# Kernel optimization log

Hardware: AMD Instinct MI355X
Metric: run time of the kernel (lower is better)

## Reference

```python
import math
import jax, jax.numpy as jnp
import numpy as np

SAMPLE_RATE = 16000
N_BANDS = 3
_F_DARK = jnp.array([270.0, 800.0, 2300.0], dtype=jnp.float32)
_F_NEUTRAL = jnp.array([500.0, 1500.0, 2500.0], dtype=jnp.float32)
_F_BRIGHT = jnp.array([730.0, 2100.0, 3000.0], dtype=jnp.float32)
_Q_DARK = jnp.array([5.0, 5.0, 5.0], dtype=jnp.float32)
_Q_NEUTRAL = jnp.array([8.0, 8.0, 8.0], dtype=jnp.float32)
_Q_BRIGHT = jnp.array([12.0, 12.0, 12.0], dtype=jnp.float32)


def _interpolate_formants(level):
    # level: [B] in [0,1] -> freqs, qs: [B, n_bands]
    t_low = jnp.clip(level * 2.0, 0.0, 1.0)[:, None]
    t_high = jnp.clip((level - 0.5) * 2.0, 0.0, 1.0)[:, None]
    use_high = (level >= 0.5)[:, None]
    freqs_lo = (1.0 - t_low) * _F_DARK + t_low * _F_NEUTRAL
    qs_lo = (1.0 - t_low) * _Q_DARK + t_low * _Q_NEUTRAL
    freqs_hi = (1.0 - t_high) * _F_NEUTRAL + t_high * _F_BRIGHT
    qs_hi = (1.0 - t_high) * _Q_NEUTRAL + t_high * _Q_BRIGHT
    freqs = jnp.where(use_high, freqs_hi, freqs_lo)
    qs = jnp.where(use_high, qs_hi, qs_lo)
    return freqs, qs


def _biquad_bandpass_coeffs(freq_hz, q):
    # freq_hz, q: [B, n_bands] -> coeffs each [B, n_bands]; b1 is 0
    omega = (2.0 * math.pi / SAMPLE_RATE) * freq_hz
    sin_o = jnp.sin(omega)
    cos_o = jnp.cos(omega)
    alpha = sin_o / (2.0 * jnp.maximum(q, 0.5))
    a0 = 1.0 + alpha
    b0 = alpha / a0
    b2 = -alpha / a0
    a1 = (-2.0 * cos_o) / a0
    a2 = (1.0 - alpha) / a0
    return b0, b2, a1, a2


def setup_inputs() -> dict:
    key = jax.random.key(0)
    k1, k2 = jax.random.split(key)
    B, S = 256, 131072
    audio = jax.random.normal(k1, (B, S), dtype=jnp.float32)
    resonance_level = jax.random.uniform(k2, (B,), dtype=jnp.float32)
    return {"audio": audio, "resonance_level": resonance_level}


def reference(audio, resonance_level):
    B, S = audio.shape
    level = jnp.clip(resonance_level.astype(audio.dtype), 0.0, 1.0)
    freqs, qs = _interpolate_formants(level)          # [B, nb]
    b0, b2, a1, a2 = _biquad_bandpass_coeffs(freqs, qs)
    # broadcast coeffs to [nb, B] for the scan
    b0, b2, a1, a2 = (c.T for c in (b0, b2, a1, a2))
    nb = N_BANDS
    zeros = jnp.zeros((nb, B), dtype=audio.dtype)
    inv_sqrt_nb = 1.0 / math.sqrt(nb)

    def step(carry, x_t):
        # carry: (x1, x2, y1, y2) each [nb, B]; x_t: [B]
        x1, x2, y1, y2 = carry
        y = b0 * x_t[None, :] + b2 * x2 - a1 * y1 - a2 * y2  # [nb, B]
        new_x1 = jnp.broadcast_to(x_t[None, :], (nb, B))
        return (new_x1, x1, y, y1), jnp.sum(y, axis=0) * inv_sqrt_nb

    _, out = jax.lax.scan(step, (zeros, zeros, zeros, zeros), audio.T)  # out: [S, B]
    return out.T
```

## Files before the change

### kernel.cpp

```cpp
#include <hip/hip_runtime.h>
#include <math.h>

#ifndef M_PI
#define M_PI 3.14159265358979323846
#endif

#define BATCHES 256
#define S_LEN   131072

#define TPB   256
#define CCH   64
#define SEGS  8
#define SEG_SAMPS (TPB * CCH)
#define WCH   16
#define WIN   (TPB + WCH)
#define PSTR  288
#define OBSTR 33

__device__ __forceinline__ void compute_coeffs(float level_in, float b0[3], float na1[3], float na2[3]) {
    const float FD[3] = {270.0f, 800.0f, 2300.0f};
    const float FN[3] = {500.0f, 1500.0f, 2500.0f};
    const float FB[3] = {730.0f, 2100.0f, 3000.0f};
    float level = fminf(fmaxf(level_in, 0.0f), 1.0f);
    float t_low  = fminf(fmaxf(level * 2.0f, 0.0f), 1.0f);
    float t_high = fminf(fmaxf((level - 0.5f) * 2.0f, 0.0f), 1.0f);
    bool hi = (level >= 0.5f);
    const float W0 = (float)(2.0 * M_PI / 16000.0);
    #pragma unroll
    for (int k = 0; k < 3; ++k) {
        float f, q;
        if (hi) { f = (1.0f - t_high) * FN[k] + t_high * FB[k];
                  q = (1.0f - t_high) * 8.0f  + t_high * 12.0f; }
        else    { f = (1.0f - t_low) * FD[k] + t_low * FN[k];
                  q = (1.0f - t_low) * 5.0f  + t_low * 8.0f; }
        float omega = W0 * f;
        float sn = sinf(omega), cs = cosf(omega);
        float alpha = sn / (2.0f * fmaxf(q, 0.5f));
        float a0 = 1.0f + alpha;
        b0[k]  = alpha / a0;
        na1[k] = (2.0f * cs) / a0;
        na2[k] = -((1.0f - alpha) / a0);
    }
}

#define STEP3(XT, XTM2, SUMV)                                                    \
    {                                                                            \
        float d = (XT) - (XTM2);                                                 \
        float e0 = fmaf(b0[0], d, na2[0] * y2[0]);                               \
        float e1 = fmaf(b0[1], d, na2[1] * y2[1]);                               \
        float e2 = fmaf(b0[2], d, na2[2] * y2[2]);                               \
        float yy0 = fmaf(na1[0], y1[0], e0);                                     \
        float yy1 = fmaf(na1[1], y1[1], e1);                                     \
        float yy2 = fmaf(na1[2], y1[2], e2);                                     \
        y2[0] = y1[0]; y1[0] = yy0;                                              \
        y2[1] = y1[1]; y1[1] = yy1;                                              \
        y2[2] = y1[2]; y1[2] = yy2;                                              \
        SUMV = (yy0 + yy1 + yy2);                                                \
    }

#define MMUL(R00,R01,R10,R11, X00,X01,X10,X11, Y00,Y01,Y10,Y11)                  \
    {                                                                            \
        R00 = X00*Y00 + X01*Y10; R01 = X00*Y01 + X01*Y11;                        \
        R10 = X10*Y00 + X11*Y10; R11 = X10*Y01 + X11*Y11;                        \
    }

__global__ __launch_bounds__(TPB, 4)
void formant_onepass(const float* __restrict__ x, const float* __restrict__ lvl,
                     float* __restrict__ out)
{
    __shared__ float lds[TPB * OBSTR];

    const int tid = threadIdx.x;
    const int row = blockIdx.x >> 3;
    const int seg = blockIdx.x & (SEGS - 1);

    float b0[3], na1[3], na2[3];
    compute_coeffs(lvl[row], b0, na1, na2);

    const float* xrow = x + (size_t)row * S_LEN;
    const size_t segBase = (size_t)seg * SEG_SAMPS;
    const float* xc = xrow + segBase + (size_t)tid * CCH;

    float xm1 = 0.f, xm2 = 0.f;
    if (seg > 0 || tid > 0) { float2 t2 = *(const float2*)(xc - 2); xm2 = t2.x; xm1 = t2.y; }

    float4 bufm[16];
    #pragma unroll
    for (int j = 0; j < 16; ++j) bufm[j] = ((const float4*)xc)[j];

    {
        float y1[3] = {0.f,0.f,0.f}, y2[3] = {0.f,0.f,0.f};
        float p1 = xm1, p2 = xm2, dummy;
        #pragma unroll
        for (int i = 0; i < 16; ++i) {
            float4 q = bufm[i];
            STEP3(q.x, p2, dummy)
            STEP3(q.y, p1, dummy)
            STEP3(q.z, q.x, dummy)
            STEP3(q.w, q.y, dummy)
            p2 = q.z; p1 = q.w;
        }
        (void)dummy;
        lds[0*PSTR + WCH + tid] = y1[0]; lds[1*PSTR + WCH + tid] = y2[0];
        lds[2*PSTR + WCH + tid] = y1[1]; lds[3*PSTR + WCH + tid] = y2[1];
        lds[4*PSTR + WCH + tid] = y1[2]; lds[5*PSTR + WCH + tid] = y2[2];
    }

    if (tid < WCH) {
        if (seg == 0) {
            #pragma unroll
            for (int e = 0; e < 6; ++e) lds[e*PSTR + tid] = 0.f;
        } else {
            const float* xw = xrow + segBase - (size_t)(WCH * CCH) + (size_t)tid * CCH;
            float2 t2 = *(const float2*)(xw - 2);
            float y1[3] = {0.f,0.f,0.f}, y2[3] = {0.f,0.f,0.f};
            float p2 = t2.x, p1 = t2.y, dummy;
            const float4* xv = (const float4*)xw;
            float4 buf[4];
            #pragma unroll
            for (int j = 0; j < 4; ++j) buf[j] = xv[j];
            #pragma unroll
            for (int i = 0; i < 16; ++i) {
                float4 q = buf[i & 3];
                if (i + 4 < 16) buf[i & 3] = xv[i + 4];
                STEP3(q.x, p2, dummy)
                STEP3(q.y, p1, dummy)
                STEP3(q.z, q.x, dummy)
                STEP3(q.w, q.y, dummy)
                p2 = q.z; p1 = q.w;
            }
            (void)dummy;
            lds[0*PSTR + tid] = y1[0]; lds[1*PSTR + tid] = y2[0];
            lds[2*PSTR + tid] = y1[1]; lds[3*PSTR + tid] = y2[1];
            lds[4*PSTR + tid] = y1[2]; lds[5*PSTR + tid] = y2[2];
        }
    }
    __syncthreads();

    {
        const int wv = tid >> 6, ln = tid & 63;
        if (wv < 3) {
            const float A1 = na1[wv], A2 = na2[wv];
            float hm1 = 1.f, hm2 = 0.f, hm3 = 0.f;
            for (int i = 0; i < CCH; ++i) {
                float h = fmaf(A1, hm1, A2 * hm2);
                hm3 = hm2; hm2 = hm1; hm1 = h;
            }
            const float H00 = hm1, H01 = A2 * hm2;
            const float H10 = hm2, H11 = A2 * hm3;

            float* z1p = lds + (2*wv) * PSTR;
            float* z2p = lds + (2*wv + 1) * PSTR;

            const int cnt = (ln < 16) ? 5 : 4;
            const int beg = (ln < 16) ? 5 * ln : 80 + 4 * (ln - 16);

            float s1 = 0.f, s2 = 0.f;
            for (int j = 0; j < cnt; ++j) {
                float z1 = z1p[beg + j], z2 = z2p[beg + j];
                float n1 = z1 + H00 * s1 + H01 * s2;
                float n2 = z2 + H10 * s1 + H11 * s2;
                s1 = n1; s2 = n2;
            }
            float B00,B01,B10,B11, C00,C01,C10,C11;
            MMUL(B00,B01,B10,B11, H00,H01,H10,H11, H00,H01,H10,H11)
            MMUL(C00,C01,C10,C11, B00,B01,B10,B11, B00,B01,B10,B11)
            float A00 = C00, A01 = C01, A10 = C10, A11 = C11;
            if (cnt == 5) {
                float D00,D01,D10,D11;
                MMUL(D00,D01,D10,D11, C00,C01,C10,C11, H00,H01,H10,H11)
                A00 = D00; A01 = D01; A10 = D10; A11 = D11;
            }
            float bb1 = s1, bb2 = s2;
            for (int d = 1; d < 64; d <<= 1) {
                float iA00 = __shfl_up(A00, d), iA01 = __shfl_up(A01, d);
                float iA10 = __shfl_up(A10, d), iA11 = __shfl_up(A11, d);
                float ib1  = __shfl_up(bb1, d), ib2  = __shfl_up(bb2, d);
                if (ln >= d) {
                    float nb1 = A00 * ib1 + A01 * ib2 + bb1;
                    float nb2 = A10 * ib1 + A11 * ib2 + bb2;
                    float n00, n01, n10, n11;
                    MMUL(n00,n01,n10,n11, A00,A01,A10,A11, iA00,iA01,iA10,iA11)
                    A00 = n00; A01 = n01; A10 = n10; A11 = n11;
                    bb1 = nb1; bb2 = nb2;
                }
            }
            float e1 = __shfl_up(bb1, 1), e2 = __shfl_up(bb2, 1);
            if (ln == 0) { e1 = 0.f; e2 = 0.f; }

            s1 = e1; s2 = e2;
            for (int j = 0; j < cnt; ++j) {
                int w = beg + j;
                float z1 = z1p[w], z2 = z2p[w];
                z1p[w] = s1; z2p[w] = s2;
                float n1 = z1 + H00 * s1 + H01 * s2;
                float n2 = z2 + H10 * s1 + H11 * s2;
                s1 = n1; s2 = n2;
            }
        }
    }
    __syncthreads();

    float y1[3], y2[3];
    y1[0] = lds[0*PSTR + WCH + tid]; y2[0] = lds[1*PSTR + WCH + tid];
    y1[1] = lds[2*PSTR + WCH + tid]; y2[1] = lds[3*PSTR + WCH + tid];
    y1[2] = lds[4*PSTR + WCH + tid]; y2[2] = lds[5*PSTR + WCH + tid];
    __syncthreads();

    {
        float p1 = xm1, p2 = xm2;
        const float is3 = 0.57735026918962576f;
        float* myob = lds + tid * OBSTR;
        float4* obase = (float4*)(out + (size_t)row * S_LEN + segBase);

        #pragma unroll
        for (int h = 0; h < 2; ++h) {
            #pragma unroll
            for (int i8 = 0; i8 < 8; ++i8) {
                float4 q = bufm[h * 8 + i8];
                float4 o;
                STEP3(q.x, p2, o.x)
                STEP3(q.y, p1, o.y)
                STEP3(q.z, q.x, o.z)
                STEP3(q.w, q.y, o.w)
                p2 = q.z; p1 = q.w;
                myob[4*i8 + 0] = o.x * is3;
                myob[4*i8 + 1] = o.y * is3;
                myob[4*i8 + 2] = o.z * is3;
                myob[4*i8 + 3] = o.w * is3;
            }
            __syncthreads();
            #pragma unroll
            for (int j = 0; j < 8; ++j) {
                int f   = j * TPB + tid;
                int ch  = f >> 3;
                int off = f & 7;
                const float* p = lds + ch * OBSTR + off * 4;
                float4 o = { p[0], p[1], p[2], p[3] };
                obase[(size_t)ch * (CCH / 4) + h * 8 + off] = o;
            }
            __syncthreads();
        }
    }
}

extern "C" void kernel_launch(void* const* d_in, const int* in_sizes, int n_in,
                              void* d_out, int out_size, void* d_ws, size_t ws_size,
                              hipStream_t stream) {
    const float* audio = (const float*)d_in[0];
    const float* level = (const float*)d_in[1];
    float* out = (float*)d_out;
    (void)in_sizes; (void)n_in; (void)d_ws; (void)ws_size; (void)out_size;

    formant_onepass<<<BATCHES * SEGS, TPB, 0, stream>>>(audio, level, out);
}
```

Before: 67.13 us.

## Stream input from global instead of holding chunk in registers to raise occupancy

Stops keeping the thread's whole 64-sample chunk in 16 float4 registers across both passes. Pass one now streams it through a 4-deep rolling buffer, and pass two reloads it from global memory in quarters (likely L2 hits). The LDS output staging is cut to quarter-size with stride 17, and launch bounds ask for 8 blocks per SM instead of 4. The aim is to lower register and LDS pressure so more waves can hide latency. The cost is reading the input twice and four sync rounds instead of two in the output phase.

Measured after the change: 100.8 us. +50.2%, slower.

```diff
diff --git a/kernel.cpp b/kernel.cpp
--- a/kernel.cpp
+++ b/kernel.cpp
@@ -13,9 +13,8 @@
 #define SEGS  8
 #define SEG_SAMPS (TPB * CCH)
 #define WCH   16
-#define WIN   (TPB + WCH)
 #define PSTR  288
-#define OBSTR 33
+#define OBSTR 17
 
 __device__ __forceinline__ void compute_coeffs(float level_in, float b0[3], float na1[3], float na2[3]) {
     const float FD[3] = {270.0f, 800.0f, 2300.0f};
@@ -64,7 +63,7 @@
         R10 = X10*Y00 + X11*Y10; R11 = X10*Y01 + X11*Y11;                        \
     }
 
-__global__ __launch_bounds__(TPB, 4)
+__global__ __launch_bounds__(TPB, 8)
 void formant_onepass(const float* __restrict__ x, const float* __restrict__ lvl,
                      float* __restrict__ out)
 {
@@ -81,19 +80,20 @@
     const size_t segBase = (size_t)seg * SEG_SAMPS;
     const float* xc = xrow + segBase + (size_t)tid * CCH;
 
-    float xm1 = 0.f, xm2 = 0.f;
-    if (seg > 0 || tid > 0) { float2 t2 = *(const float2*)(xc - 2); xm2 = t2.x; xm1 = t2.y; }
-
-    float4 bufm[16];
-    #pragma unroll
-    for (int j = 0; j < 16; ++j) bufm[j] = ((const float4*)xc)[j];
+    float xm1_0 = 0.f, xm2_0 = 0.f;
+    if (seg > 0 || tid > 0) { float2 t2 = *(const float2*)(xc - 2); xm2_0 = t2.x; xm1_0 = t2.y; }
 
     {
         float y1[3] = {0.f,0.f,0.f}, y2[3] = {0.f,0.f,0.f};
-        float p1 = xm1, p2 = xm2, dummy;
+        float p1 = xm1_0, p2 = xm2_0, dummy;
+        const float4* xv = (const float4*)xc;
+        float4 buf[4];
+        #pragma unroll
+        for (int j = 0; j < 4; ++j) buf[j] = xv[j];
         #pragma unroll
         for (int i = 0; i < 16; ++i) {
-            float4 q = bufm[i];
+            float4 q = buf[i & 3];
+            if (i + 4 < 16) buf[i & 3] = xv[i + 4];
             STEP3(q.x, p2, dummy)
             STEP3(q.y, p1, dummy)
             STEP3(q.z, q.x, dummy)
@@ -208,36 +208,40 @@
     __syncthreads();
 
     {
-        float p1 = xm1, p2 = xm2;
+        float p1 = xm1_0, p2 = xm2_0;
         const float is3 = 0.57735026918962576f;
+        const float4* xv = (const float4*)xc;
         float* myob = lds + tid * OBSTR;
         float4* obase = (float4*)(out + (size_t)row * S_LEN + segBase);
 
         #pragma unroll
-        for (int h = 0; h < 2; ++h) {
-            #pragma unroll
-            for (int i8 = 0; i8 < 8; ++i8) {
-                float4 q = bufm[h * 8 + i8];
+        for (int qr = 0; qr < 4; ++qr) {
+            float4 xq[4];
+            #pragma unroll
+            for (int i = 0; i < 4; ++i) xq[i] = xv[qr * 4 + i];
+            #pragma unroll
+            for (int i = 0; i < 4; ++i) {
+                float4 q = xq[i];
                 float4 o;
                 STEP3(q.x, p2, o.x)
                 STEP3(q.y, p1, o.y)
                 STEP3(q.z, q.x, o.z)
                 STEP3(q.w, q.y, o.w)
                 p2 = q.z; p1 = q.w;
-                myob[4*i8 + 0] = o.x * is3;
-                myob[4*i8 + 1] = o.y * is3;
-                myob[4*i8 + 2] = o.z * is3;
-                myob[4*i8 + 3] = o.w * is3;
+                myob[4*i + 0] = o.x * is3;
+                myob[4*i + 1] = o.y * is3;
+                myob[4*i + 2] = o.z * is3;
+                myob[4*i + 3] = o.w * is3;
             }
             __syncthreads();
             #pragma unroll
-            for (int j = 0; j < 8; ++j) {
+            for (int j = 0; j < 4; ++j) {
                 int f   = j * TPB + tid;
-                int ch  = f >> 3;
-                int off = f & 7;
+                int ch  = f >> 2;
+                int off = f & 3;
                 const float* p = lds + ch * OBSTR + off * 4;
                 float4 o = { p[0], p[1], p[2], p[3] };
-                obase[(size_t)ch * (CCH / 4) + h * 8 + off] = o;
+                obase[(size_t)ch * (CCH / 4) + qr * 4 + off] = o;
             }
             __syncthreads();
         }
```

## Reuse zero-state outputs and add carry correction via impulse response

Applied to the files above, without the earlier changes.

Cuts the chunk length to 32 and doubles the segments per row. The first pass now stores the zero-initial-state filtered outputs in LDS. The final pass no longer re-runs the recurrence; it adds the carried-in state's contribution using a precomputed impulse-response table per band, built by the scan waves. This removes the second serial filtering pass and the large per-thread input register buffer, at the cost of more LDS traffic and a longer warm-up window.

Result: faster. 58.91 us (-12.2%).

```diff
diff --git a/kernel.cpp b/kernel.cpp
--- a/kernel.cpp
+++ b/kernel.cpp
@@ -9,13 +9,16 @@
 #define S_LEN   131072
 
 #define TPB   256
-#define CCH   64
-#define SEGS  8
+#define CCH   32
+#define SEGS  16
 #define SEG_SAMPS (TPB * CCH)
-#define WCH   16
-#define WIN   (TPB + WCH)
-#define PSTR  288
+#define WCH   24
+#define NCH   (TPB + WCH)
 #define OBSTR 33
+#define SCAN_OFF 8448
+#define SCAN_STR 281
+#define H_OFF 10136
+#define LDSF  10232
 
 __device__ __forceinline__ void compute_coeffs(float level_in, float b0[3], float na1[3], float na2[3]) {
     const float FD[3] = {270.0f, 800.0f, 2300.0f};
@@ -68,10 +71,10 @@
 void formant_onepass(const float* __restrict__ x, const float* __restrict__ lvl,
                      float* __restrict__ out)
 {
-    __shared__ float lds[TPB * OBSTR];
+    __shared__ float lds[LDSF];
 
     const int tid = threadIdx.x;
-    const int row = blockIdx.x >> 3;
+    const int row = blockIdx.x >> 4;
     const int seg = blockIdx.x & (SEGS - 1);
 
     float b0[3], na1[3], na2[3];
@@ -81,35 +84,42 @@
     const size_t segBase = (size_t)seg * SEG_SAMPS;
     const float* xc = xrow + segBase + (size_t)tid * CCH;
 
-    float xm1 = 0.f, xm2 = 0.f;
-    if (seg > 0 || tid > 0) { float2 t2 = *(const float2*)(xc - 2); xm2 = t2.x; xm1 = t2.y; }
-
-    float4 bufm[16];
-    #pragma unroll
-    for (int j = 0; j < 16; ++j) bufm[j] = ((const float4*)xc)[j];
-
     {
+        float xm1 = 0.f, xm2 = 0.f;
+        if (seg > 0 || tid > 0) { float2 t2 = *(const float2*)(xc - 2); xm2 = t2.x; xm1 = t2.y; }
         float y1[3] = {0.f,0.f,0.f}, y2[3] = {0.f,0.f,0.f};
-        float p1 = xm1, p2 = xm2, dummy;
+        const float4* xv = (const float4*)xc;
+        float* myob = lds + tid * OBSTR;
+        float4 buf[4];
         #pragma unroll
-        for (int i = 0; i < 16; ++i) {
-            float4 q = bufm[i];
-            STEP3(q.x, p2, dummy)
-            STEP3(q.y, p1, dummy)
-            STEP3(q.z, q.x, dummy)
-            STEP3(q.w, q.y, dummy)
-            p2 = q.z; p1 = q.w;
-        }
-        (void)dummy;
-        lds[0*PSTR + WCH + tid] = y1[0]; lds[1*PSTR + WCH + tid] = y2[0];
-        lds[2*PSTR + WCH + tid] = y1[1]; lds[3*PSTR + WCH + tid] = y2[1];
-        lds[4*PSTR + WCH + tid] = y1[2]; lds[5*PSTR + WCH + tid] = y2[2];
+        for (int j = 0; j < 4; ++j) buf[j] = xv[j];
+        #pragma unroll
+        for (int i = 0; i < 8; ++i) {
+            float4 q = buf[i & 3];
+            if (i + 4 < 8) buf[i & 3] = xv[i + 4];
+            float4 o;
+            STEP3(q.x, xm2, o.x)
+            STEP3(q.y, xm1, o.y)
+            STEP3(q.z, q.x, o.z)
+            STEP3(q.w, q.y, o.w)
+            xm2 = q.z; xm1 = q.w;
+            myob[4*i + 0] = o.x;
+            myob[4*i + 1] = o.y;
+            myob[4*i + 2] = o.z;
+            myob[4*i + 3] = o.w;
+        }
+        lds[SCAN_OFF + 0*SCAN_STR + WCH + tid] = y1[0];
+        lds[SCAN_OFF + 1*SCAN_STR + WCH + tid] = y2[0];
+        lds[SCAN_OFF + 2*SCAN_STR + WCH + tid] = y1[1];
+        lds[SCAN_OFF + 3*SCAN_STR + WCH + tid] = y2[1];
+        lds[SCAN_OFF + 4*SCAN_STR + WCH + tid] = y1[2];
+        lds[SCAN_OFF + 5*SCAN_STR + WCH + tid] = y2[2];
     }
 
     if (tid < WCH) {
         if (seg == 0) {
             #pragma unroll
-            for (int e = 0; e < 6; ++e) lds[e*PSTR + tid] = 0.f;
+            for (int e = 0; e < 6; ++e) lds[SCAN_OFF + e*SCAN_STR + tid] = 0.f;
         } else {
             const float* xw = xrow + segBase - (size_t)(WCH * CCH) + (size_t)tid * CCH;
             float2 t2 = *(const float2*)(xw - 2);
@@ -120,9 +130,9 @@
             #pragma unroll
             for (int j = 0; j < 4; ++j) buf[j] = xv[j];
             #pragma unroll
-            for (int i = 0; i < 16; ++i) {
+            for (int i = 0; i < 8; ++i) {
                 float4 q = buf[i & 3];
-                if (i + 4 < 16) buf[i & 3] = xv[i + 4];
+                if (i + 4 < 8) buf[i & 3] = xv[i + 4];
                 STEP3(q.x, p2, dummy)
                 STEP3(q.y, p1, dummy)
                 STEP3(q.z, q.x, dummy)
@@ -130,9 +140,12 @@
                 p2 = q.z; p1 = q.w;
             }
             (void)dummy;
-            lds[0*PSTR + tid] = y1[0]; lds[1*PSTR + tid] = y2[0];
-            lds[2*PSTR + tid] = y1[1]; lds[3*PSTR + tid] = y2[1];
-            lds[4*PSTR + tid] = y1[2]; lds[5*PSTR + tid] = y2[2];
+            lds[SCAN_OFF + 0*SCAN_STR + tid] = y1[0];
+            lds[SCAN_OFF + 1*SCAN_STR + tid] = y2[0];
+            lds[SCAN_OFF + 2*SCAN_STR + tid] = y1[1];
+            lds[SCAN_OFF + 3*SCAN_STR + tid] = y2[1];
+            lds[SCAN_OFF + 4*SCAN_STR + tid] = y1[2];
+            lds[SCAN_OFF + 5*SCAN_STR + tid] = y2[2];
         }
     }
     __syncthreads();
@@ -145,15 +158,16 @@
             for (int i = 0; i < CCH; ++i) {
                 float h = fmaf(A1, hm1, A2 * hm2);
                 hm3 = hm2; hm2 = hm1; hm1 = h;
+                if (ln == 0) lds[H_OFF + wv * CCH + i] = h;
             }
             const float H00 = hm1, H01 = A2 * hm2;
             const float H10 = hm2, H11 = A2 * hm3;
 
-            float* z1p = lds + (2*wv) * PSTR;
-            float* z2p = lds + (2*wv + 1) * PSTR;
-
-            const int cnt = (ln < 16) ? 5 : 4;
-            const int beg = (ln < 16) ? 5 * ln : 80 + 4 * (ln - 16);
+            float* z1p = lds + SCAN_OFF + (2*wv) * SCAN_STR;
+            float* z2p = lds + SCAN_OFF + (2*wv + 1) * SCAN_STR;
+
+            const int cnt = (ln < 24) ? 5 : 4;
+            const int beg = (ln < 24) ? 5 * ln : 120 + 4 * (ln - 24);
 
             float s1 = 0.f, s2 = 0.f;
             for (int j = 0; j < cnt; ++j) {
@@ -201,45 +215,30 @@
     }
     __syncthreads();
 
-    float y1[3], y2[3];
-    y1[0] = lds[0*PSTR + WCH + tid]; y2[0] = lds[1*PSTR + WCH + tid];
-    y1[1] = lds[2*PSTR + WCH + tid]; y2[1] = lds[3*PSTR + WCH + tid];
-    y1[2] = lds[4*PSTR + WCH + tid]; y2[2] = lds[5*PSTR + WCH + tid];
-    __syncthreads();
-
     {
-        float p1 = xm1, p2 = xm2;
         const float is3 = 0.57735026918962576f;
-        float* myob = lds + tid * OBSTR;
         float4* obase = (float4*)(out + (size_t)row * S_LEN + segBase);
-
         #pragma unroll
-        for (int h = 0; h < 2; ++h) {
-            #pragma unroll
-            for (int i8 = 0; i8 < 8; ++i8) {
-                float4 q = bufm[h * 8 + i8];
-                float4 o;
-                STEP3(q.x, p2, o.x)
-                STEP3(q.y, p1, o.y)
-                STEP3(q.z, q.x, o.z)
-                STEP3(q.w, q.y, o.w)
-                p2 = q.z; p1 = q.w;
-                myob[4*i8 + 0] = o.x * is3;
-                myob[4*i8 + 1] = o.y * is3;
-                myob[4*i8 + 2] = o.z * is3;
-                myob[4*i8 + 3] = o.w * is3;
-            }
-            __syncthreads();
-            #pragma unroll
-            for (int j = 0; j < 8; ++j) {
-                int f   = j * TPB + tid;
-                int ch  = f >> 3;
-                int off = f & 7;
-                const float* p = lds + ch * OBSTR + off * 4;
-                float4 o = { p[0], p[1], p[2], p[3] };
-                obase[(size_t)ch * (CCH / 4) + h * 8 + off] = o;
-            }
-            __syncthreads();
+        for (int j = 0; j < 8; ++j) {
+            const int f   = j * TPB + tid;
+            const int ch  = f >> 3;
+            const int off = f & 7;
+            const int t   = off * 4;
+            const float* sp = lds + ch * OBSTR + t;
+            float o0 = sp[0], o1 = sp[1], o2 = sp[2], o3 = sp[3];
+            #pragma unroll
+            for (int k = 0; k < 3; ++k) {
+                const float c1 = lds[SCAN_OFF + (2*k)   * SCAN_STR + WCH + ch];
+                const float c2 = na2[k] * lds[SCAN_OFF + (2*k+1) * SCAN_STR + WCH + ch];
+                const float4 hv = *(const float4*)&lds[H_OFF + k * CCH + t];
+                const float hm = (off == 0) ? 1.0f : lds[H_OFF + k * CCH + t - 1];
+                o0 = fmaf(c1, hv.x, fmaf(c2, hm,   o0));
+                o1 = fmaf(c1, hv.y, fmaf(c2, hv.x, o1));
+                o2 = fmaf(c1, hv.z, fmaf(c2, hv.y, o2));
+                o3 = fmaf(c1, hv.w, fmaf(c2, hv.z, o3));
+            }
+            float4 o = { o0 * is3, o1 * is3, o2 * is3, o3 * is3 };
+            obase[f] = o;
         }
     }
 }
```
